# Performance work log

Measured on AMD Instinct MI355X. Metric: run time of the kernel, lower is better.

Reference implementation:

```python
import jax, jax.numpy as jnp
import numpy as np

B, N, C = 4, 2048, 3
IN_DIM, OUT_DIM, H = 128, 128, 4
D = OUT_DIM // H  # d_head = 32
NEG_INF = -1e9


def setup_inputs() -> dict:
    key = jax.random.key(0)
    k_h, k_adj, k_W, k_a, k_Wo, k_bo = jax.random.split(key, 6)
    h = jax.random.normal(k_h, (B, N, IN_DIM), dtype=jnp.float32)
    adj = jax.random.normal(k_adj, (B, C, N, N), dtype=jnp.float32)
    # params (xavier-ish scales)
    W = jax.random.normal(k_W, (IN_DIM, OUT_DIM), dtype=jnp.float32) * (1.0 / np.sqrt(IN_DIM))
    a = jax.random.normal(k_a, (H, 2 * D), dtype=jnp.float32) * (1.0 / np.sqrt(2 * D))
    a_src, a_dst = a[:, :D], a[:, D:]
    Wo = jax.random.normal(k_Wo, (OUT_DIM, OUT_DIM), dtype=jnp.float32) * (1.0 / np.sqrt(OUT_DIM))
    bo = jnp.zeros((OUT_DIM,), dtype=jnp.float32)
    return {"h": h, "adj": adj, "W": W, "a_src": a_src, "a_dst": a_dst, "Wo": Wo, "bo": bo}


def reference(h, adj, W, a_src, a_dst, Wo, bo):
    b, n, _ = h.shape
    # Wh: [B, N, H, D]
    Wh = jnp.einsum('bni,io->bno', h, W).reshape(b, n, H, D)
    # additive attention score decomposed: e[b,h,i,j] = lrelu(a_src.Wh_i + a_dst.Wh_j)
    src = jnp.einsum('bnhd,hd->bhn', Wh, a_src)  # [B,H,N]
    dst = jnp.einsum('bnhd,hd->bhn', Wh, a_dst)  # [B,H,N]
    e = jax.nn.leaky_relu(src[:, :, :, None] + dst[:, :, None, :], negative_slope=0.2)  # [B,H,N,N]
    # mask from multi-channel adjacency: [B,1,N,N]
    mask = (jnp.mean(adj, axis=1, keepdims=True) > 0).astype(e.dtype)
    e = e * mask + (1.0 - mask) * NEG_INF
    alpha = jax.nn.softmax(e, axis=-1)  # dropout is identity in eval mode
    # weighted sum over j: out[b,i,h,d] = sum_j alpha[b,h,i,j] * Wh[b,j,h,d]
    out = jnp.einsum('bhij,bjhd->bihd', alpha, Wh).reshape(b, n, OUT_DIM)
    return jax.nn.elu(out @ Wo + bo)
```

## Files before the change

kernel.cpp:

```cpp
#include <hip/hip_runtime.h>
#include <math.h>

#define BB 4
#define NN 2048
#define CC 3
#define HH 4
#define DD 32

__global__ __launch_bounds__(256) void k1_wh(const float* __restrict__ h,
                                             const float* __restrict__ W,
                                             const float* __restrict__ a_src,
                                             const float* __restrict__ a_dst,
                                             float* __restrict__ Wh,
                                             float* __restrict__ srcv,
                                             float* __restrict__ dstv) {
    __shared__ float hrow[2][128];
    int tid = threadIdx.x;
    int r = tid >> 7, c = tid & 127;
    int row = blockIdx.x * 2 + r;
    int b = row >> 11;
    int n = row & 2047;
    hrow[r][c] = h[row * 128 + c];
    __syncthreads();
    float acc = 0.f;
#pragma unroll
    for (int k = 0; k < 128; ++k)
        acc = fmaf(hrow[r][k], W[k * 128 + c], acc);
    Wh[row * 128 + c] = acc;
    float ps = acc * a_src[c];
    float pd = acc * a_dst[c];
#pragma unroll
    for (int m = 16; m >= 1; m >>= 1) {
        ps += __shfl_xor(ps, m);
        pd += __shfl_xor(pd, m);
    }
    if ((c & 31) == 0) {
        int hh = c >> 5;
        srcv[(b * HH + hh) * NN + n] = ps;
        dstv[(b * HH + hh) * NN + n] = pd;
    }
}

__global__ __launch_bounds__(256) void k2_mask(const float* __restrict__ adj,
                                               const float* __restrict__ dstv,
                                               unsigned long long* __restrict__ maskbits,
                                               float* __restrict__ dmax) {
    __shared__ float dl[HH][NN];
    int tid = threadIdx.x;
    int rowg0 = blockIdx.x * 4;
    int b = rowg0 >> 11;
    for (int idx = tid; idx < HH * NN; idx += 256) {
        int hh = idx >> 11, j = idx & 2047;
        dl[hh][j] = dstv[(b * HH + hh) * NN + j];
    }
    __syncthreads();
    int wave = tid >> 6, lane = tid & 63;
    int i = (rowg0 & 2047) + wave;
    const float* a0 = adj + ((long long)(b * CC + 0) * NN + i) * NN;
    const float* a1 = adj + ((long long)(b * CC + 1) * NN + i) * NN;
    const float* a2 = adj + ((long long)(b * CC + 2) * NN + i) * NN;
    float m0 = -INFINITY, m1 = -INFINITY, m2 = -INFINITY, m3 = -INFINITY;
#pragma unroll 4
    for (int jt = 0; jt < NN / 64; ++jt) {
        int j = jt * 64 + lane;
        float s = a0[j] + a1[j] + a2[j];
        bool bit = s > 0.f;
        unsigned long long mw = __ballot(bit);
        if (lane == 0) maskbits[((long long)b * NN + i) * 32 + jt] = mw;
        float d0v = bit ? dl[0][j] : -INFINITY;
        float d1v = bit ? dl[1][j] : -INFINITY;
        float d2v = bit ? dl[2][j] : -INFINITY;
        float d3v = bit ? dl[3][j] : -INFINITY;
        m0 = fmaxf(m0, d0v);
        m1 = fmaxf(m1, d1v);
        m2 = fmaxf(m2, d2v);
        m3 = fmaxf(m3, d3v);
    }
#pragma unroll
    for (int m = 32; m >= 1; m >>= 1) {
        m0 = fmaxf(m0, __shfl_xor(m0, m));
        m1 = fmaxf(m1, __shfl_xor(m1, m));
        m2 = fmaxf(m2, __shfl_xor(m2, m));
        m3 = fmaxf(m3, __shfl_xor(m3, m));
    }
    if (lane == 0) {
        dmax[(b * HH + 0) * NN + i] = m0;
        dmax[(b * HH + 1) * NN + i] = m1;
        dmax[(b * HH + 2) * NN + i] = m2;
        dmax[(b * HH + 3) * NN + i] = m3;
    }
}

__global__ __launch_bounds__(256) void k3_attn(const float* __restrict__ Wh,
                                               const float* __restrict__ srcv,
                                               const float* __restrict__ dstv,
                                               const float* __restrict__ dmax,
                                               const unsigned long long* __restrict__ maskbits,
                                               float* __restrict__ part,
                                               float* __restrict__ plsum) {
    __shared__ __align__(16) float wh_lds[2][64 * 32];
    __shared__ __align__(16) float p_lds[4][16 * 65];
    int tid = threadIdx.x;
    int wave = tid >> 6, lane = tid & 63;
    int blk = blockIdx.x;
    int jh = blk & 1;
    int rest = blk >> 1;
    int it = rest & 31;
    int bh = rest >> 5;
    int b = bh >> 2, hh = bh & 3;
    int row_base = it * 64 + wave * 16;
    int rgrp = lane >> 3, dgrp = lane & 7;
    int r0 = rgrp * 2, d0 = dgrp * 4;
    int jt0 = jh * 16;
    long long bhN = (long long)(b * HH + hh) * NN;
    const float* whbase = Wh + (long long)b * NN * 128 + hh * 32;

    float srcR[16], mR[16];
    bool amR[16];
#pragma unroll
    for (int r = 0; r < 16; ++r) {
        int row = row_base + r;
        float s = srcv[bhN + row];
        float dm = dmax[bhN + row];
        bool allm = !(dm > -INFINITY);
        float e = s + dm;
        float lr = e > 0.f ? e : 0.2f * e;
        srcR[r] = s;
        mR[r] = allm ? 0.f : lr;
        amR[r] = allm;
    }

    int f4a = tid, f4b = 256 + tid;
    int ja = f4a >> 3, da = (f4a & 7) * 4;
    int jb = f4b >> 3, db = (f4b & 7) * 4;

    {
        int j0 = jt0 * 64;
        float4 s0 = *(const float4*)&whbase[(long long)(j0 + ja) * 128 + da];
        float4 s1 = *(const float4*)&whbase[(long long)(j0 + jb) * 128 + db];
        *(float4*)&wh_lds[0][ja * 32 + da] = s0;
        *(float4*)&wh_lds[0][jb * 32 + db] = s1;
    }
    __syncthreads();

    float acc[2][4] = {{0.f, 0.f, 0.f, 0.f}, {0.f, 0.f, 0.f, 0.f}};
    float lsum[2] = {0.f, 0.f};
    float* pw = p_lds[wave];
    float dv = dstv[bhN + jt0 * 64 + lane];

    for (int t = 0; t < 16; ++t) {
        int jt = jt0 + t;
        int cur = t & 1;
        bool hasnext = (t < 15);
        float4 n0, n1;
        float dvn = 0.f;
        if (hasnext) {
            int jn0 = (jt + 1) * 64;
            n0 = *(const float4*)&whbase[(long long)(jn0 + ja) * 128 + da];
            n1 = *(const float4*)&whbase[(long long)(jn0 + jb) * 128 + db];
            dvn = dstv[bhN + jn0 + lane];
        }
        const unsigned long long* mrow =
            maskbits + ((long long)b * NN + row_base) * 32 + jt;
#pragma unroll
        for (int r = 0; r < 16; ++r) {
            unsigned long long mw = mrow[r * 32];
            bool bit = (mw >> lane) & 1ull;
            float e = srcR[r] + dv;
            float lr = e > 0.f ? e : 0.2f * e;
            float p = amR[r] ? 1.f : (bit ? __expf(lr - mR[r]) : 0.f);
            pw[r * 65 + lane] = p;
        }
        const float* whc = wh_lds[cur];
#pragma unroll 4
        for (int j = 0; j < 64; ++j) {
            const float4 w4 = *(const float4*)&whc[j * 32 + d0];
            float p0 = pw[r0 * 65 + j];
            float p1 = pw[r0 * 65 + 65 + j];
            acc[0][0] = fmaf(p0, w4.x, acc[0][0]);
            acc[0][1] = fmaf(p0, w4.y, acc[0][1]);
            acc[0][2] = fmaf(p0, w4.z, acc[0][2]);
            acc[0][3] = fmaf(p0, w4.w, acc[0][3]);
            acc[1][0] = fmaf(p1, w4.x, acc[1][0]);
            acc[1][1] = fmaf(p1, w4.y, acc[1][1]);
            acc[1][2] = fmaf(p1, w4.z, acc[1][2]);
            acc[1][3] = fmaf(p1, w4.w, acc[1][3]);
            lsum[0] += p0;
            lsum[1] += p1;
        }
        if (hasnext) {
            *(float4*)&wh_lds[cur ^ 1][ja * 32 + da] = n0;
            *(float4*)&wh_lds[cur ^ 1][jb * 32 + db] = n1;
            dv = dvn;
        }
        __syncthreads();
    }

#pragma unroll
    for (int rr = 0; rr < 2; ++rr) {
        int row_local = wave * 16 + r0 + rr;
        float4 o;
        o.x = acc[rr][0];
        o.y = acc[rr][1];
        o.z = acc[rr][2];
        o.w = acc[rr][3];
        *(float4*)&part[((long long)blk * 64 + row_local) * 32 + d0] = o;
        if (dgrp == 0) plsum[blk * 64 + row_local] = lsum[rr];
    }
}

__global__ __launch_bounds__(256) void k3_reduce(const float* __restrict__ part,
                                                 const float* __restrict__ plsum,
                                                 float* __restrict__ attn) {
    int g = blockIdx.x * 256 + threadIdx.x;
    int d4 = g & 7;
    int r = (g >> 3) & 63;
    int it = (g >> 9) & 31;
    int bh = g >> 14;
    int b = bh >> 2, hh = bh & 3;
    int tile0 = (bh * 32 + it) * 2;
    const float4 p0 = *(const float4*)&part[((long long)tile0 * 64 + r) * 32 + d4 * 4];
    const float4 p1 = *(const float4*)&part[((long long)(tile0 + 1) * 64 + r) * 32 + d4 * 4];
    float l = plsum[tile0 * 64 + r] + plsum[(tile0 + 1) * 64 + r];
    float inv = 1.f / l;
    float4 o;
    o.x = (p0.x + p1.x) * inv;
    o.y = (p0.y + p1.y) * inv;
    o.z = (p0.z + p1.z) * inv;
    o.w = (p0.w + p1.w) * inv;
    int n = it * 64 + r;
    *(float4*)&attn[((long long)(b * NN + n) * 128) + hh * 32 + d4 * 4] = o;
}

__global__ __launch_bounds__(256) void k4_out(const float* __restrict__ attn,
                                              const float* __restrict__ Wo,
                                              const float* __restrict__ bo,
                                              float* __restrict__ out) {
    __shared__ float arow[2][128];
    int tid = threadIdx.x;
    int r = tid >> 7, c = tid & 127;
    int row = blockIdx.x * 2 + r;
    arow[r][c] = attn[row * 128 + c];
    __syncthreads();
    float acc = bo[c];
#pragma unroll
    for (int k = 0; k < 128; ++k)
        acc = fmaf(arow[r][k], Wo[k * 128 + c], acc);
    out[row * 128 + c] = acc > 0.f ? acc : expm1f(acc);
}

extern "C" void kernel_launch(void* const* d_in, const int* in_sizes, int n_in,
                              void* d_out, int out_size, void* d_ws, size_t ws_size,
                              hipStream_t stream) {
    const float* h     = (const float*)d_in[0];
    const float* adj   = (const float*)d_in[1];
    const float* W     = (const float*)d_in[2];
    const float* a_src = (const float*)d_in[3];
    const float* a_dst = (const float*)d_in[4];
    const float* Wo    = (const float*)d_in[5];
    const float* bo    = (const float*)d_in[6];
    float* out = (float*)d_out;

    char* ws = (char*)d_ws;
    float* Wh   = (float*)(ws);
    float* attn = (float*)(ws + (4 << 20));
    float* srcv = (float*)(ws + (8 << 20));
    float* dstv = (float*)(ws + (8 << 20) + (128 << 10));
    float* dmax = (float*)(ws + (8 << 20) + (256 << 10));
    unsigned long long* maskbits =
        (unsigned long long*)(ws + (8 << 20) + (384 << 10));
    float* part  = (float*)(ws + (10 << 20) + (384 << 10));
    float* plsum = (float*)(ws + (18 << 20) + (384 << 10));

    k1_wh<<<dim3(BB * NN / 2), dim3(256), 0, stream>>>(h, W, a_src, a_dst, Wh, srcv, dstv);
    k2_mask<<<dim3(BB * NN / 4), dim3(256), 0, stream>>>(adj, dstv, maskbits, dmax);
    k3_attn<<<dim3(BB * HH * (NN / 64) * 2), dim3(256), 0, stream>>>(Wh, srcv, dstv, dmax,
                                                                     maskbits, part, plsum);
    k3_reduce<<<dim3(1024), dim3(256), 0, stream>>>(part, plsum, attn);
    k4_out<<<dim3(BB * NN / 2), dim3(256), 0, stream>>>(attn, Wo, bo, out);
}
```

Before: 447.4 us.

## Use bf16 MFMA for attention aggregation with transposed bf16 Wh and vectorized mask

Replaces the scalar-FMA LDS-tiled attention accumulation with bf16 MFMA 16x16x32 instructions. A new kernel transposes Wh into a bf16 per-head [d][j] layout to act as the B operand. The mask kernel now reads adj with float4 loads and packs 32-bit mask words. This removes LDS traffic and syncs from the attention stage, at the cost of bf16 rounding of probabilities and Wh plus an extra transpose launch.

```diff
diff --git a/kernel.cpp b/kernel.cpp
--- a/kernel.cpp
+++ b/kernel.cpp
@@ -1,4 +1,5 @@
 #include <hip/hip_runtime.h>
+#include <hip/hip_bf16.h>
 #include <math.h>
 
 #define BB 4
@@ -6,6 +7,14 @@
 #define CC 3
 #define HH 4
 #define DD 32
+
+typedef __attribute__((ext_vector_type(8))) short bf16x8;
+typedef __attribute__((ext_vector_type(4))) float f32x4;
+
+__device__ inline unsigned short f2bf(float x) {
+    __hip_bfloat16 b = __float2bfloat16(x);
+    return __builtin_bit_cast(unsigned short, b);
+}
 
 __global__ __launch_bounds__(256) void k1_wh(const float* __restrict__ h,
                                              const float* __restrict__ W,
@@ -41,17 +50,37 @@
     }
 }
 
+__global__ __launch_bounds__(256) void k1t(const float* __restrict__ Wh,
+                                           unsigned short* __restrict__ WhT) {
+    int tid = threadIdx.x;
+    int wave = tid >> 6, lane = tid & 63;
+    int blk = blockIdx.x;
+    int jb = blk & 15;
+    int dgrp = (blk >> 4) & 1;
+    int bh = blk >> 5;
+    int b = bh >> 2, hh = bh & 3;
+    int d = dgrp * 16 + (lane & 15);
+    int jc = jb * 128 + wave * 32 + (lane >> 4) * 8;
+    const float* src = Wh + ((long long)(b * NN + jc)) * 128 + hh * 32 + d;
+    bf16x8 v;
+#pragma unroll
+    for (int i = 0; i < 8; ++i)
+        v[i] = (short)f2bf(src[i * 128]);
+    *(bf16x8*)&WhT[((long long)bh * 32 + d) * NN + jc] = v;
+}
+
 __global__ __launch_bounds__(256) void k2_mask(const float* __restrict__ adj,
                                                const float* __restrict__ dstv,
-                                               unsigned long long* __restrict__ maskbits,
+                                               unsigned* __restrict__ maskb32,
                                                float* __restrict__ dmax) {
     __shared__ float dl[HH][NN];
     int tid = threadIdx.x;
     int rowg0 = blockIdx.x * 4;
     int b = rowg0 >> 11;
-    for (int idx = tid; idx < HH * NN; idx += 256) {
-        int hh = idx >> 11, j = idx & 2047;
-        dl[hh][j] = dstv[(b * HH + hh) * NN + j];
+    {
+        const float4* s4 = (const float4*)(dstv + (long long)b * HH * NN);
+        float4* d4 = (float4*)&dl[0][0];
+        for (int idx = tid; idx < HH * NN / 4; idx += 256) d4[idx] = s4[idx];
     }
     __syncthreads();
     int wave = tid >> 6, lane = tid & 63;
@@ -60,21 +89,33 @@
     const float* a1 = adj + ((long long)(b * CC + 1) * NN + i) * NN;
     const float* a2 = adj + ((long long)(b * CC + 2) * NN + i) * NN;
     float m0 = -INFINITY, m1 = -INFINITY, m2 = -INFINITY, m3 = -INFINITY;
-#pragma unroll 4
-    for (int jt = 0; jt < NN / 64; ++jt) {
-        int j = jt * 64 + lane;
-        float s = a0[j] + a1[j] + a2[j];
-        bool bit = s > 0.f;
-        unsigned long long mw = __ballot(bit);
-        if (lane == 0) maskbits[((long long)b * NN + i) * 32 + jt] = mw;
-        float d0v = bit ? dl[0][j] : -INFINITY;
-        float d1v = bit ? dl[1][j] : -INFINITY;
-        float d2v = bit ? dl[2][j] : -INFINITY;
-        float d3v = bit ? dl[3][j] : -INFINITY;
-        m0 = fmaxf(m0, d0v);
-        m1 = fmaxf(m1, d1v);
-        m2 = fmaxf(m2, d2v);
-        m3 = fmaxf(m3, d3v);
+    for (int jt = 0; jt < 8; ++jt) {
+        int j4 = jt * 256 + lane * 4;
+        float4 f0 = *(const float4*)&a0[j4];
+        float4 f1 = *(const float4*)&a1[j4];
+        float4 f2 = *(const float4*)&a2[j4];
+        unsigned nib = (unsigned)(f0.x + f1.x + f2.x > 0.f) |
+                       ((unsigned)(f0.y + f1.y + f2.y > 0.f) << 1) |
+                       ((unsigned)(f0.z + f1.z + f2.z > 0.f) << 2) |
+                       ((unsigned)(f0.w + f1.w + f2.w > 0.f) << 3);
+        unsigned w = nib << (4 * (lane & 7));
+        w |= __shfl_xor((int)w, 1);
+        w |= __shfl_xor((int)w, 2);
+        w |= __shfl_xor((int)w, 4);
+        if ((lane & 7) == 0) maskb32[((long long)b * NN + i) * 64 + (j4 >> 5)] = w;
+#pragma unroll
+        for (int hh = 0; hh < HH; ++hh) {
+            float4 dv4 = ((const float4*)&dl[hh][0])[jt * 64 + lane];
+            float a = (nib & 1) ? dv4.x : -INFINITY;
+            float bb2 = (nib & 2) ? dv4.y : -INFINITY;
+            float cc2 = (nib & 4) ? dv4.z : -INFINITY;
+            float dd2 = (nib & 8) ? dv4.w : -INFINITY;
+            float mx = fmaxf(fmaxf(a, bb2), fmaxf(cc2, dd2));
+            if (hh == 0) m0 = fmaxf(m0, mx);
+            if (hh == 1) m1 = fmaxf(m1, mx);
+            if (hh == 2) m2 = fmaxf(m2, mx);
+            if (hh == 3) m3 = fmaxf(m3, mx);
+        }
     }
 #pragma unroll
     for (int m = 32; m >= 1; m >>= 1) {
@@ -91,15 +132,13 @@
     }
 }
 
-__global__ __launch_bounds__(256) void k3_attn(const float* __restrict__ Wh,
+__global__ __launch_bounds__(256) void k3_attn(const unsigned short* __restrict__ WhT,
                                                const float* __restrict__ srcv,
                                                const float* __restrict__ dstv,
                                                const float* __restrict__ dmax,
-                                               const unsigned long long* __restrict__ maskbits,
+                                               const unsigned* __restrict__ maskb32,
                                                float* __restrict__ part,
                                                float* __restrict__ plsum) {
-    __shared__ __align__(16) float wh_lds[2][64 * 32];
-    __shared__ __align__(16) float p_lds[4][16 * 65];
     int tid = threadIdx.x;
     int wave = tid >> 6, lane = tid & 63;
     int blk = blockIdx.x;
@@ -107,106 +146,60 @@
     int rest = blk >> 1;
     int it = rest & 31;
     int bh = rest >> 5;
-    int b = bh >> 2, hh = bh & 3;
-    int row_base = it * 64 + wave * 16;
-    int rgrp = lane >> 3, dgrp = lane & 7;
-    int r0 = rgrp * 2, d0 = dgrp * 4;
-    int jt0 = jh * 16;
-    long long bhN = (long long)(b * HH + hh) * NN;
-    const float* whbase = Wh + (long long)b * NN * 128 + hh * 32;
-
-    float srcR[16], mR[16];
-    bool amR[16];
-#pragma unroll
-    for (int r = 0; r < 16; ++r) {
-        int row = row_base + r;
-        float s = srcv[bhN + row];
-        float dm = dmax[bhN + row];
-        bool allm = !(dm > -INFINITY);
-        float e = s + dm;
-        float lr = e > 0.f ? e : 0.2f * e;
-        srcR[r] = s;
-        mR[r] = allm ? 0.f : lr;
-        amR[r] = allm;
-    }
-
-    int f4a = tid, f4b = 256 + tid;
-    int ja = f4a >> 3, da = (f4a & 7) * 4;
-    int jb = f4b >> 3, db = (f4b & 7) * 4;
-
-    {
-        int j0 = jt0 * 64;
-        float4 s0 = *(const float4*)&whbase[(long long)(j0 + ja) * 128 + da];
-        float4 s1 = *(const float4*)&whbase[(long long)(j0 + jb) * 128 + db];
-        *(float4*)&wh_lds[0][ja * 32 + da] = s0;
-        *(float4*)&wh_lds[0][jb * 32 + db] = s1;
-    }
-    __syncthreads();
-
-    float acc[2][4] = {{0.f, 0.f, 0.f, 0.f}, {0.f, 0.f, 0.f, 0.f}};
-    float lsum[2] = {0.f, 0.f};
-    float* pw = p_lds[wave];
-    float dv = dstv[bhN + jt0 * 64 + lane];
-
-    for (int t = 0; t < 16; ++t) {
-        int jt = jt0 + t;
-        int cur = t & 1;
-        bool hasnext = (t < 15);
-        float4 n0, n1;
-        float dvn = 0.f;
-        if (hasnext) {
-            int jn0 = (jt + 1) * 64;
-            n0 = *(const float4*)&whbase[(long long)(jn0 + ja) * 128 + da];
-            n1 = *(const float4*)&whbase[(long long)(jn0 + jb) * 128 + db];
-            dvn = dstv[bhN + jn0 + lane];
+    int b = bh >> 2;
+    int r = lane & 15, kg = lane >> 4;
+    long long bhN = (long long)bh * NN;
+    int row = it * 64 + wave * 16 + r;
+
+    float s = srcv[bhN + row];
+    float dm = dmax[bhN + row];
+    bool allm = !(dm > -INFINITY);
+    float e0 = s + dm;
+    float m = e0 > 0.f ? e0 : 0.2f * e0;
+    if (allm) m = 0.f;
+
+    const unsigned* mrow = maskb32 + ((long long)b * NN + row) * 64;
+    const unsigned short* wb = WhT + (long long)bh * 32 * NN;
+    const unsigned short* w0 = wb + (long long)r * NN;
+    const unsigned short* w1 = wb + (long long)(16 + r) * NN;
+
+    f32x4 acc0 = {0.f, 0.f, 0.f, 0.f};
+    f32x4 acc1 = {0.f, 0.f, 0.f, 0.f};
+    float psum = 0.f;
+
+    for (int t = 0; t < 32; ++t) {
+        unsigned mw = mrow[jh * 32 + t];
+        int jk = jh * 1024 + t * 32 + kg * 8;
+        float4 dva = *(const float4*)&dstv[bhN + jk];
+        float4 dvb = *(const float4*)&dstv[bhN + jk + 4];
+        float dvs[8] = {dva.x, dva.y, dva.z, dva.w, dvb.x, dvb.y, dvb.z, dvb.w};
+        bf16x8 af;
+#pragma unroll
+        for (int i = 0; i < 8; ++i) {
+            float e = s + dvs[i];
+            float lr = e > 0.f ? e : 0.2f * e;
+            bool bit = (mw >> (kg * 8 + i)) & 1u;
+            float p = allm ? 1.f : (bit ? __expf(lr - m) : 0.f);
+            psum += p;
+            af[i] = (short)f2bf(p);
         }
-        const unsigned long long* mrow =
-            maskbits + ((long long)b * NN + row_base) * 32 + jt;
-#pragma unroll
-        for (int r = 0; r < 16; ++r) {
-            unsigned long long mw = mrow[r * 32];
-            bool bit = (mw >> lane) & 1ull;
-            float e = srcR[r] + dv;
-            float lr = e > 0.f ? e : 0.2f * e;
-            float p = amR[r] ? 1.f : (bit ? __expf(lr - mR[r]) : 0.f);
-            pw[r * 65 + lane] = p;
-        }
-        const float* whc = wh_lds[cur];
-#pragma unroll 4
-        for (int j = 0; j < 64; ++j) {
-            const float4 w4 = *(const float4*)&whc[j * 32 + d0];
-            float p0 = pw[r0 * 65 + j];
-            float p1 = pw[r0 * 65 + 65 + j];
-            acc[0][0] = fmaf(p0, w4.x, acc[0][0]);
-            acc[0][1] = fmaf(p0, w4.y, acc[0][1]);
-            acc[0][2] = fmaf(p0, w4.z, acc[0][2]);
-            acc[0][3] = fmaf(p0, w4.w, acc[0][3]);
-            acc[1][0] = fmaf(p1, w4.x, acc[1][0]);
-            acc[1][1] = fmaf(p1, w4.y, acc[1][1]);
-            acc[1][2] = fmaf(p1, w4.z, acc[1][2]);
-            acc[1][3] = fmaf(p1, w4.w, acc[1][3]);
-            lsum[0] += p0;
-            lsum[1] += p1;
-        }
-        if (hasnext) {
-            *(float4*)&wh_lds[cur ^ 1][ja * 32 + da] = n0;
-            *(float4*)&wh_lds[cur ^ 1][jb * 32 + db] = n1;
-            dv = dvn;
-        }
-        __syncthreads();
-    }
-
-#pragma unroll
-    for (int rr = 0; rr < 2; ++rr) {
-        int row_local = wave * 16 + r0 + rr;
-        float4 o;
-        o.x = acc[rr][0];
-        o.y = acc[rr][1];
-        o.z = acc[rr][2];
-        o.w = acc[rr][3];
-        *(float4*)&part[((long long)blk * 64 + row_local) * 32 + d0] = o;
-        if (dgrp == 0) plsum[blk * 64 + row_local] = lsum[rr];
-    }
+        bf16x8 bf0 = *(const bf16x8*)&w0[jk];
+        bf16x8 bf1 = *(const bf16x8*)&w1[jk];
+        acc0 = __builtin_amdgcn_mfma_f32_16x16x32_bf16(af, bf0, acc0, 0, 0, 0);
+        acc1 = __builtin_amdgcn_mfma_f32_16x16x32_bf16(af, bf1, acc1, 0, 0, 0);
+    }
+
+    psum += __shfl_xor(psum, 16);
+    psum += __shfl_xor(psum, 32);
+
+    long long pbase = (long long)blk * 64 + wave * 16;
+#pragma unroll
+    for (int reg = 0; reg < 4; ++reg) {
+        int rl = kg * 4 + reg;
+        part[(pbase + rl) * 32 + r] = acc0[reg];
+        part[(pbase + rl) * 32 + 16 + r] = acc1[reg];
+    }
+    if (kg == 0) plsum[pbase + r] = psum;
 }
 
 __global__ __launch_bounds__(256) void k3_reduce(const float* __restrict__ part,
@@ -262,20 +255,21 @@
     float* out = (float*)d_out;
 
     char* ws = (char*)d_ws;
-    float* Wh   = (float*)(ws);
-    float* attn = (float*)(ws + (4 << 20));
-    float* srcv = (float*)(ws + (8 << 20));
-    float* dstv = (float*)(ws + (8 << 20) + (128 << 10));
-    float* dmax = (float*)(ws + (8 << 20) + (256 << 10));
-    unsigned long long* maskbits =
-        (unsigned long long*)(ws + (8 << 20) + (384 << 10));
+    float* Wh    = (float*)(ws);
+    float* attn  = (float*)(ws + (4 << 20));
+    float* srcv  = (float*)(ws + (8 << 20));
+    float* dstv  = (float*)(ws + (8 << 20) + (128 << 10));
+    float* dmax  = (float*)(ws + (8 << 20) + (256 << 10));
+    unsigned* maskb32 = (unsigned*)(ws + (8 << 20) + (384 << 10));
     float* part  = (float*)(ws + (10 << 20) + (384 << 10));
     float* plsum = (float*)(ws + (18 << 20) + (384 << 10));
+    unsigned short* WhT = (unsigned short*)(ws + (18 << 20) + (640 << 10));
 
     k1_wh<<<dim3(BB * NN / 2), dim3(256), 0, stream>>>(h, W, a_src, a_dst, Wh, srcv, dstv);
-    k2_mask<<<dim3(BB * NN / 4), dim3(256), 0, stream>>>(adj, dstv, maskbits, dmax);
-    k3_attn<<<dim3(BB * HH * (NN / 64) * 2), dim3(256), 0, stream>>>(Wh, srcv, dstv, dmax,
-                                                                     maskbits, part, plsum);
+    k1t<<<dim3(512), dim3(256), 0, stream>>>(Wh, WhT);
+    k2_mask<<<dim3(BB * NN / 4), dim3(256), 0, stream>>>(adj, dstv, maskb32, dmax);
+    k3_attn<<<dim3(BB * HH * (NN / 64) * 2), dim3(256), 0, stream>>>(WhT, srcv, dstv, dmax,
+                                                                     maskb32, part, plsum);
     k3_reduce<<<dim3(1024), dim3(256), 0, stream>>>(part, plsum, attn);
     k4_out<<<dim3(BB * NN / 2), dim3(256), 0, stream>>>(attn, Wo, bo, out);
 }
```

Result: faster. 390.2 us (-12.8%).
